# Kernel tuning notes

Hardware: AMD Instinct MI355X
Metric: run time of the kernel (lower is better)

Reference implementation:

```python
import jax, jax.numpy as jnp
import numpy as np

EMB = 768
HEADS = 12
HEAD_DIM = EMB // HEADS
SEQ = 4096
BATCH = 1


def setup_inputs() -> dict:
    key = jax.random.key(0)
    ks = jax.random.split(key, 9)
    s = 1.0 / np.sqrt(EMB)
    return {
        "x": jax.random.normal(ks[0], (BATCH, SEQ, EMB), dtype=jnp.float32),
        "wq": jax.random.normal(ks[1], (EMB, EMB), dtype=jnp.float32) * s,
        "bq": jax.random.normal(ks[2], (EMB,), dtype=jnp.float32) * s,
        "wk": jax.random.normal(ks[3], (EMB, EMB), dtype=jnp.float32) * s,
        "bk": jax.random.normal(ks[4], (EMB,), dtype=jnp.float32) * s,
        "wv": jax.random.normal(ks[5], (EMB, EMB), dtype=jnp.float32) * s,
        "bv": jax.random.normal(ks[6], (EMB,), dtype=jnp.float32) * s,
        "wo": jax.random.normal(ks[7], (EMB, EMB), dtype=jnp.float32) * s,
        "bo": jax.random.normal(ks[8], (EMB,), dtype=jnp.float32) * s,
    }


def reference(x, wq, bq, wk, bk, wv, bv, wo, bo):
    b, n, _ = x.shape
    # projections: [b, n, emb] -> [b, heads, n, head_dim]
    def split_heads(t):
        return t.reshape(b, n, HEADS, HEAD_DIM).transpose(0, 2, 1, 3)
    q = split_heads(x @ wq + bq)
    k = split_heads(x @ wk + bk)
    v = split_heads(x @ wv + bv)
    # full N x N scores (naive attention, as in the original)
    scores = jnp.einsum("bhqd,bhkd->bhqk", q, k)
    causal = jnp.triu(jnp.ones((n, n), dtype=bool), k=1)
    scores = jnp.where(causal, -jnp.inf, scores)
    weights = jax.nn.softmax(scores / np.sqrt(HEAD_DIM), axis=-1)
    # dropout with rate 0.0 is identity (eval mode)
    ctx = jnp.einsum("bhqk,bhkd->bhqd", weights, v)
    ctx = ctx.transpose(0, 2, 1, 3).reshape(b, n, EMB)
    return ctx @ wo + bo
```

## Files before the change

kernel.cpp:

```cpp
#include <hip/hip_runtime.h>
#include <stdint.h>

#define SEQ 4096
#define EMB 768
#define HEADS 12
#define HD 64

typedef __attribute__((ext_vector_type(8))) short short8;
typedef __attribute__((ext_vector_type(4))) short short4v;
typedef __attribute__((ext_vector_type(8))) __bf16 bf16x8;
typedef __attribute__((ext_vector_type(4))) __bf16 bf16x4;
typedef __attribute__((ext_vector_type(4))) float f32x4;

#define QSCALE 0.18033688011112043f

static __device__ __forceinline__ unsigned short f2bf(float f) {
    unsigned int u = __builtin_bit_cast(unsigned int, f);
    unsigned int r = 0x7fffu + ((u >> 16) & 1u);
    u += r;
    return (unsigned short)(u >> 16);
}

static __device__ __forceinline__ f32x4 mfma32(short8 a, short8 b, f32x4 c) {
    return __builtin_amdgcn_mfma_f32_16x16x32_bf16(
        __builtin_bit_cast(bf16x8, a), __builtin_bit_cast(bf16x8, b), c, 0, 0, 0);
}

static __device__ __forceinline__ f32x4 mfma16(short4v a, short4v b, f32x4 c) {
#if __has_builtin(__builtin_amdgcn_mfma_f32_16x16x16_bf16)
    return __builtin_amdgcn_mfma_f32_16x16x16_bf16(
        __builtin_bit_cast(bf16x4, a), __builtin_bit_cast(bf16x4, b), c, 0, 0, 0);
#else
    return __builtin_amdgcn_mfma_f32_16x16x16bf16_1k(a, b, c, 0, 0, 0);
#endif
}

static __device__ __forceinline__ short4v pack4bf(float a, float b, float c, float d) {
#if __has_builtin(__builtin_amdgcn_cvt_pk_bf16_f32)
    typedef __attribute__((ext_vector_type(2))) __bf16 bf16x2;
    bf16x2 lo = __builtin_amdgcn_cvt_pk_bf16_f32(a, b);
    bf16x2 hi = __builtin_amdgcn_cvt_pk_bf16_f32(c, d);
    uint2 u = {__builtin_bit_cast(unsigned int, lo), __builtin_bit_cast(unsigned int, hi)};
    return __builtin_bit_cast(short4v, u);
#else
    short4v p;
    p[0] = (short)f2bf(a); p[1] = (short)f2bf(b);
    p[2] = (short)f2bf(c); p[3] = (short)f2bf(d);
    return p;
#endif
}

static __device__ __forceinline__ void load_lds16(const void* g, void* l) {
    __builtin_amdgcn_global_load_lds(
        (const __attribute__((address_space(1))) unsigned int*)(uintptr_t)g,
        (__attribute__((address_space(3))) unsigned int*)(uintptr_t)l, 16, 0, 0);
}

static __device__ __forceinline__ int pid_of(int h, int i128, int ch) {
    int b = (i128 < 20) ? (i128 - 10)
                        : (i128 < 30 ? 10 + (i128 - 20) * 2 : 30 + (i128 - 30) * 3);
    return h * 36 + b + (ch - 1);
}

static __device__ __forceinline__ void softmax_step(f32x4* st, float& m_i, float& l_i,
                                                    f32x4* O, short4v* pk) {
    float t0 = fmaxf(fmaxf(st[0][0], st[0][1]), fmaxf(st[0][2], st[0][3]));
    float t1 = fmaxf(fmaxf(st[1][0], st[1][1]), fmaxf(st[1][2], st[1][3]));
    float t2 = fmaxf(fmaxf(st[2][0], st[2][1]), fmaxf(st[2][2], st[2][3]));
    float t3 = fmaxf(fmaxf(st[3][0], st[3][1]), fmaxf(st[3][2], st[3][3]));
    float mx = fmaxf(fmaxf(t0, t1), fmaxf(t2, t3));
    mx = fmaxf(mx, __shfl_xor(mx, 16));
    mx = fmaxf(mx, __shfl_xor(mx, 32));
    if (__ballot(mx > m_i + 5.0f)) {
        const bool inc = mx > m_i;
        const float mn = inc ? mx : m_i;
        const float alpha = __builtin_amdgcn_exp2f(m_i - mn);
        m_i = mn;
        l_i *= alpha;
        for (int dt = 0; dt < 4; dt++)
            for (int r = 0; r < 4; r++) O[dt][r] *= alpha;
    }
    float rs = 0.f;
    for (int nt = 0; nt < 4; nt++) {
        float p0 = __builtin_amdgcn_exp2f(st[nt][0] - m_i);
        float p1 = __builtin_amdgcn_exp2f(st[nt][1] - m_i);
        float p2 = __builtin_amdgcn_exp2f(st[nt][2] - m_i);
        float p3 = __builtin_amdgcn_exp2f(st[nt][3] - m_i);
        rs += p0 + p1 + p2 + p3;
        pk[nt] = pack4bf(p0, p1, p2, p3);
    }
    l_i += rs;
}

__global__ __launch_bounds__(256) void convert_all(const float* __restrict__ x,
                                                   const float* __restrict__ wq,
                                                   const float* __restrict__ wk,
                                                   const float* __restrict__ wv,
                                                   const float* __restrict__ wo,
                                                   unsigned short* __restrict__ xb,
                                                   unsigned short* __restrict__ wqkvT,
                                                   unsigned short* __restrict__ woT) {
    __shared__ float Ls[64][65];
    const int bid = blockIdx.x;
    if (bid < 3072) {
        int i = bid * 256 + threadIdx.x;
        float4 v = ((const float4*)x)[i];
        ushort4 o = {f2bf(v.x), f2bf(v.y), f2bf(v.z), f2bf(v.w)};
        ((ushort4*)xb)[i] = o;
        return;
    }
    const int idx = bid - 3072;
    const int z = idx / 144;
    const int bx = (idx % 144) / 12, by = idx % 12;
    const float* W = (z == 0) ? wq : (z == 1) ? wk : (z == 2) ? wv : wo;
    unsigned short* dst = (z < 3) ? (wqkvT + (size_t)z * EMB * EMB) : woT;
    const int k0 = bx * 64, n0 = by * 64;
    const int r = threadIdx.x >> 2, c0 = (threadIdx.x & 3) * 16;
    for (int j = 0; j < 16; j += 4) {
        float4 v = *(const float4*)&W[(size_t)(k0 + r) * EMB + n0 + c0 + j];
        Ls[r][c0 + j] = v.x;
        Ls[r][c0 + j + 1] = v.y;
        Ls[r][c0 + j + 2] = v.z;
        Ls[r][c0 + j + 3] = v.w;
    }
    __syncthreads();
    unsigned short tmp[16];
    for (int j = 0; j < 16; j++) tmp[j] = f2bf(Ls[c0 + j][r]);
    *(uint4*)&dst[(size_t)(n0 + r) * EMB + k0 + c0] = *(uint4*)tmp;
    *(uint4*)&dst[(size_t)(n0 + r) * EMB + k0 + c0 + 8] = *(uint4*)(tmp + 8);
}

__global__ __launch_bounds__(256) void gemm_qkv(const unsigned short* __restrict__ A,
                                                const unsigned short* __restrict__ Bt,
                                                const float* __restrict__ b0p,
                                                const float* __restrict__ b1p,
                                                const float* __restrict__ b2p,
                                                unsigned short* __restrict__ QKb,
                                                unsigned short* __restrict__ Vtb) {
    __shared__ __align__(16) unsigned short SMEM[16384];
    const int tid = threadIdx.x;
    const int wave = tid >> 6, lane = tid & 63, quad = lane >> 4, l16 = lane & 15;
    const int m0 = blockIdx.x * 128, n0 = blockIdx.y * 128;
    const int wm = (wave >> 1) * 64, wn = (wave & 1) * 64;
    const int lrow = lane >> 2, lcol = (lane & 3) * 8;

    f32x4 acc[4][4] = {};

    for (int t = 0; t < 2; t++) {
        int row = wave * 32 + t * 16 + lrow;
        load_lds16(&A[(size_t)(m0 + row) * EMB + lcol], &SMEM[(wave * 2 + t) * 512]);
        load_lds16(&Bt[(size_t)(n0 + row) * EMB + lcol], &SMEM[4096 + (wave * 2 + t) * 512]);
    }
    int buf = 0;
    for (int k0 = 0; k0 < EMB; k0 += 32) {
        __syncthreads();
        if (k0 + 32 < EMB) {
            unsigned short* A_ = &SMEM[(buf ^ 1) * 8192];
            unsigned short* B_ = A_ + 4096;
            for (int t = 0; t < 2; t++) {
                int row = wave * 32 + t * 16 + lrow;
                load_lds16(&A[(size_t)(m0 + row) * EMB + k0 + 32 + lcol], &A_[(wave * 2 + t) * 512]);
                load_lds16(&Bt[(size_t)(n0 + row) * EMB + k0 + 32 + lcol], &B_[(wave * 2 + t) * 512]);
            }
        }
        const unsigned short* A_ = &SMEM[buf * 8192];
        const unsigned short* B_ = A_ + 4096;
        short8 a[4], b[4];
        for (int i = 0; i < 4; i++) a[i] = *(const short8*)&A_[(wm + i * 16 + l16) * 32 + quad * 8];
        for (int i = 0; i < 4; i++) b[i] = *(const short8*)&B_[(wn + i * 16 + l16) * 32 + quad * 8];
        for (int i = 0; i < 4; i++)
            for (int j = 0; j < 4; j++) acc[i][j] = mfma32(a[i], b[j], acc[i][j]);
        buf ^= 1;
    }

    const int z = n0 / EMB;
    if (z < 2) {
        const float* bias = z ? b1p : b0p;
        const float sc = z ? 1.0f : QSCALE;
        for (int i = 0; i < 4; i++)
            for (int j = 0; j < 4; j++) {
                int mbase = m0 + wm + i * 16 + quad * 4;
                int n = n0 + wn + j * 16 + l16;
                float bv = bias[n - z * EMB];
                for (int r = 0; r < 4; r++)
                    QKb[(size_t)(mbase + r) * 1536 + n] = f2bf((acc[i][j][r] + bv) * sc);
            }
    } else {
        const int nn = n0 + wn + l16 - 2 * EMB;
        for (int j = 0; j < 4; j++) {
            __syncthreads();
            const float bv = b2p[nn + j * 16];
            const int nloc = (wave & 1) * 16 + l16;
            for (int i = 0; i < 4; i++) {
                ushort4 pk;
                pk.x = f2bf(acc[i][j][0] + bv);
                pk.y = f2bf(acc[i][j][1] + bv);
                pk.z = f2bf(acc[i][j][2] + bv);
                pk.w = f2bf(acc[i][j][3] + bv);
                *(ushort4*)&SMEM[nloc * 136 + wm + i * 16 + quad * 4] = pk;
            }
            __syncthreads();
            const int nl = tid >> 3, c = tid & 7;
            const int ng = (nl >> 4) * 64 + j * 16 + (nl & 15) + n0 - 2 * EMB;
            const int hh = ng >> 6, dd = ng & 63;
            unsigned short* dst = &Vtb[(size_t)(hh * HD + dd) * SEQ + m0];
            *(uint4*)&dst[c * 8] = *(uint4*)&SMEM[nl * 136 + c * 8];
            *(uint4*)&dst[64 + c * 8] = *(uint4*)&SMEM[nl * 136 + 64 + c * 8];
        }
    }
}

__global__ __launch_bounds__(256) void gemm_out(const unsigned short* __restrict__ A,
                                                const unsigned short* __restrict__ Bt,
                                                const float* __restrict__ bias,
                                                float* __restrict__ outp) {
    __shared__ __align__(16) unsigned short SMEM[12288];
    const int tid = threadIdx.x;
    const int wave = tid >> 6, lane = tid & 63, quad = lane >> 4, l16 = lane & 15;
    const int m0 = blockIdx.x * 64, n0 = blockIdx.y * 128;
    const int wm = (wave >> 1) * 32, wn = (wave & 1) * 64;
    const int lrow = lane >> 2, lcol = (lane & 3) * 8;

    f32x4 acc[2][4] = {};

    load_lds16(&A[(size_t)(m0 + wave * 16 + lrow) * EMB + lcol], &SMEM[wave * 512]);
    for (int t = 0; t < 2; t++) {
        int row = wave * 32 + t * 16 + lrow;
        load_lds16(&Bt[(size_t)(n0 + row) * EMB + lcol], &SMEM[4096 + (wave * 2 + t) * 512]);
    }
    int buf = 0;
    for (int k0 = 0; k0 < EMB; k0 += 32) {
        __syncthreads();
        if (k0 + 32 < EMB) {
            unsigned short* A_ = &SMEM[(buf ^ 1) * 2048];
            unsigned short* B_ = &SMEM[4096 + (buf ^ 1) * 4096];
            load_lds16(&A[(size_t)(m0 + wave * 16 + lrow) * EMB + k0 + 32 + lcol], &A_[wave * 512]);
            for (int t = 0; t < 2; t++) {
                int row = wave * 32 + t * 16 + lrow;
                load_lds16(&Bt[(size_t)(n0 + row) * EMB + k0 + 32 + lcol], &B_[(wave * 2 + t) * 512]);
            }
        }
        const unsigned short* A_ = &SMEM[buf * 2048];
        const unsigned short* B_ = &SMEM[4096 + buf * 4096];
        short8 a[2], b[4];
        for (int i = 0; i < 2; i++) a[i] = *(const short8*)&A_[(wm + i * 16 + l16) * 32 + quad * 8];
        for (int j = 0; j < 4; j++) b[j] = *(const short8*)&B_[(wn + j * 16 + l16) * 32 + quad * 8];
        for (int i = 0; i < 2; i++)
            for (int j = 0; j < 4; j++) acc[i][j] = mfma32(a[i], b[j], acc[i][j]);
        buf ^= 1;
    }

    for (int i = 0; i < 2; i++)
        for (int j = 0; j < 4; j++) {
            int mbase = m0 + wm + i * 16 + quad * 4;
            int n = n0 + wn + j * 16 + l16;
            float bv = bias[n];
            for (int r = 0; r < 4; r++) outp[(size_t)(mbase + r) * EMB + n] = acc[i][j][r] + bv;
        }
}

__global__ __launch_bounds__(512) void attn_kernel(const unsigned short* __restrict__ QKb,
                                                   const unsigned short* __restrict__ Vtb,
                                                   unsigned short* __restrict__ ctxb,
                                                   unsigned short* __restrict__ Op,
                                                   float* __restrict__ mArr,
                                                   float* __restrict__ lArr) {
    __shared__ __align__(16) unsigned short Ks[2][64 * 64];
    __shared__ __align__(16) unsigned short Vs[2][64 * 64];

    const int bid = blockIdx.x;
    const int h = bid % HEADS;
    const int r2 = 67 - bid / HEADS;
    int i128, ch, nch;
    if (r2 < 10) {
        i128 = r2; ch = 0; nch = 1;
    } else if (r2 < 30) {
        int t = r2 - 10; i128 = 10 + (t >> 1); ch = t & 1; nch = 2;
    } else if (r2 < 60) {
        int t = r2 - 30; i128 = 20 + t / 3; ch = t % 3; nch = 3;
    } else {
        int t = r2 - 60; i128 = 30 + (t >> 2); ch = t & 3; nch = 4;
    }
    const int T = 2 * i128 + 2;
    const int kb = ch * T / nch;
    const int ke = (ch + 1) * T / nch - 1;
    const int qbase = i128 * 128;
    const int tid = threadIdx.x;
    const int wave = tid >> 6, lane = tid & 63, quad = lane >> 4, l16 = lane & 15;

    const unsigned short* Qg = QKb + (size_t)h * HD;
    const unsigned short* Kg = QKb + (size_t)(EMB + h * HD);
    const unsigned short* Vh = Vtb + (size_t)h * HD * SEQ;

    const int q = qbase + wave * 16 + l16;
    const short8 bQ0 = *(const short8*)&Qg[(size_t)q * 1536 + quad * 8];
    const short8 bQ1 = *(const short8*)&Qg[(size_t)q * 1536 + 32 + quad * 8];

    const int row = tid >> 3, t8 = tid & 7;
    const int swk = row & 7, swv = row & 15;

    f32x4 O[4] = {};
    float m_i = -3.0e38f, l_i = 0.f;

    uint4 kr, vr;
    {
        const int kb64 = kb * 64;
        kr = *(const uint4*)&Kg[(size_t)(kb64 + row) * 1536 + t8 * 8];
        vr = *(const uint4*)&Vh[(size_t)row * SEQ + kb64 + t8 * 8];
    }
    *(uint4*)&Ks[0][row * 64 + (t8 ^ swk) * 8] = kr;
    *(uint2*)&Vs[0][row * 64 + ((2 * t8) ^ swv) * 4] = ((const uint2*)&vr)[0];
    *(uint2*)&Vs[0][row * 64 + ((2 * t8 + 1) ^ swv) * 4] = ((const uint2*)&vr)[1];
    if (kb < ke) {
        const int nb = (kb + 1) * 64;
        kr = *(const uint4*)&Kg[(size_t)(nb + row) * 1536 + t8 * 8];
        vr = *(const uint4*)&Vh[(size_t)row * SEQ + nb + t8 * 8];
    }
    __syncthreads();

    const int qw = qbase + wave * 16 + 15;
    int p = 0;
    for (int kt = kb; kt <= ke; kt++) {
        const int kbase = kt * 64;
        if (kt < ke) {
            const int pn = p ^ 1;
            *(uint4*)&Ks[pn][row * 64 + (t8 ^ swk) * 8] = kr;
            *(uint2*)&Vs[pn][row * 64 + ((2 * t8) ^ swv) * 4] = ((const uint2*)&vr)[0];
            *(uint2*)&Vs[pn][row * 64 + ((2 * t8 + 1) ^ swv) * 4] = ((const uint2*)&vr)[1];
            if (kt + 1 < ke) {
                const int nb = (kt + 2) * 64;
                kr = *(const uint4*)&Kg[(size_t)(nb + row) * 1536 + t8 * 8];
                vr = *(const uint4*)&Vh[(size_t)row * SEQ + nb + t8 * 8];
            }
        }

        if (kbase <= qw) {
            const int swr = l16 & 7;
            f32x4 st[4];
            for (int nt = 0; nt < 4; nt++) {
                short8 aK0 = *(const short8*)&Ks[p][(nt * 16 + l16) * 64 + (quad ^ swr) * 8];
                short8 aK1 = *(const short8*)&Ks[p][(nt * 16 + l16) * 64 + ((quad + 4) ^ swr) * 8];
                f32x4 z = {};
                z = mfma32(aK0, bQ0, z);
                z = mfma32(aK1, bQ1, z);
                st[nt] = z;
            }
            if (kbase + 63 > qbase + wave * 16) {
                for (int nt = 0; nt < 4; nt++)
                    for (int r = 0; r < 4; r++)
                        if (kbase + nt * 16 + quad * 4 + r > q) st[nt][r] = -INFINITY;
            }

            short4v pk[4];
            softmax_step(st, m_i, l_i, O, pk);

            for (int dt = 0; dt < 4; dt++)
                for (int nt = 0; nt < 4; nt++) {
                    short4v av =
                        *(const short4v*)&Vs[p][(dt * 16 + l16) * 64 + ((4 * nt + quad) ^ l16) * 4];
                    O[dt] = mfma16(av, pk[nt], O[dt]);
                }
        }

        __syncthreads();
        p ^= 1;
    }

    l_i += __shfl_xor(l_i, 16);
    l_i += __shfl_xor(l_i, 32);

    const int ql = wave * 16 + l16;
    if (nch == 1) {
        const float inv = 1.f / l_i;
        for (int dt = 0; dt < 4; dt++) {
            ushort4 o;
            o.x = f2bf(O[dt][0] * inv);
            o.y = f2bf(O[dt][1] * inv);
            o.z = f2bf(O[dt][2] * inv);
            o.w = f2bf(O[dt][3] * inv);
            *(ushort4*)&ctxb[(size_t)q * EMB + h * HD + dt * 16 + quad * 4] = o;
        }
    } else {
        if (ch == 0) {
            for (int dt = 0; dt < 4; dt++) {
                ushort4 o;
                o.x = f2bf(O[dt][0]);
                o.y = f2bf(O[dt][1]);
                o.z = f2bf(O[dt][2]);
                o.w = f2bf(O[dt][3]);
                *(ushort4*)&ctxb[(size_t)q * EMB + h * HD + dt * 16 + quad * 4] = o;
            }
        } else {
            const int pid = pid_of(h, i128, ch);
            for (int dt = 0; dt < 4; dt++) {
                ushort4 o;
                o.x = f2bf(O[dt][0]);
                o.y = f2bf(O[dt][1]);
                o.z = f2bf(O[dt][2]);
                o.w = f2bf(O[dt][3]);
                *(ushort4*)&Op[(size_t)pid * 8192 + ql * 64 + dt * 16 + quad * 4] = o;
            }
        }
        if (quad == 0) {
            const int mli = ((h * 32 + i128) * 4 + ch) * 128 + ql;
            mArr[mli] = m_i;
            lArr[mli] = l_i;
        }
    }
}

__global__ __launch_bounds__(256) void merge_kernel(const unsigned short* __restrict__ Op,
                                                    const float* __restrict__ mArr,
                                                    const float* __restrict__ lArr,
                                                    unsigned short* __restrict__ ctxb) {
    const int gid = blockIdx.x;
    const int h = gid % HEADS;
    const int i128 = 10 + gid / HEADS;
    const int nch = (i128 < 20) ? 2 : (i128 < 30) ? 3 : 4;
    const int q = threadIdx.x >> 1, d0 = (threadIdx.x & 1) * 32;
    const int mlbase = (h * 32 + i128) * 4;

    float mc[4], lc[4];
    for (int c = 0; c < nch; c++) {
        mc[c] = mArr[(mlbase + c) * 128 + q];
        lc[c] = lArr[(mlbase + c) * 128 + q];
    }
    float M = mc[0];
    for (int c = 1; c < nch; c++) M = fmaxf(M, mc[c]);
    float w[4], L = 0.f;
    for (int c = 0; c < nch; c++) {
        w[c] = __builtin_amdgcn_exp2f(mc[c] - M);
        L += w[c] * lc[c];
    }
    const float inv = 1.f / L;
    for (int c = 0; c < nch; c++) w[c] *= inv;

    unsigned short* dst = &ctxb[(size_t)(i128 * 128 + q) * EMB + h * HD + d0];
    for (int jj = 0; jj < 32; jj += 8) {
        uint4 u0 = *(const uint4*)&dst[jj];
        float f[8];
        const unsigned short* p0 = (const unsigned short*)&u0;
        for (int t = 0; t < 8; t++)
            f[t] = w[0] * __builtin_bit_cast(float, (unsigned int)p0[t] << 16);
        for (int c = 1; c < nch; c++) {
            const int pid = pid_of(h, i128, c);
            uint4 u = *(const uint4*)&Op[(size_t)pid * 8192 + q * 64 + d0 + jj];
            const unsigned short* p = (const unsigned short*)&u;
            for (int t = 0; t < 8; t++)
                f[t] += w[c] * __builtin_bit_cast(float, (unsigned int)p[t] << 16);
        }
        unsigned short o[8];
        for (int t = 0; t < 8; t++) o[t] = f2bf(f[t]);
        *(uint4*)&dst[jj] = *(uint4*)o;
    }
}

extern "C" void kernel_launch(void* const* d_in, const int* in_sizes, int n_in,
                              void* d_out, int out_size, void* d_ws, size_t ws_size,
                              hipStream_t stream) {
    const float* x = (const float*)d_in[0];
    const float* wq = (const float*)d_in[1];
    const float* bq = (const float*)d_in[2];
    const float* wk = (const float*)d_in[3];
    const float* bk = (const float*)d_in[4];
    const float* wv = (const float*)d_in[5];
    const float* bv = (const float*)d_in[6];
    const float* wo = (const float*)d_in[7];
    const float* bo = (const float*)d_in[8];

    unsigned short* ws = (unsigned short*)d_ws;
    unsigned short* xb = ws;
    unsigned short* wqkvT = xb + SEQ * EMB;
    unsigned short* woT = wqkvT + 3 * EMB * EMB;
    unsigned short* QKb = woT + EMB * EMB;
    unsigned short* Vtb = QKb + (size_t)SEQ * 1536;
    unsigned short* ctxb = Vtb + HEADS * SEQ * HD;
    unsigned short* Op = xb;
    float* mArr = (float*)(ws + 3538944);
    float* lArr = mArr + 196608;

    convert_all<<<dim3(3072 + 576), 256, 0, stream>>>(x, wq, wk, wv, wo, xb, wqkvT, woT);
    gemm_qkv<<<dim3(SEQ / 128, 3 * EMB / 128), 256, 0, stream>>>(
        xb, wqkvT, bq, bk, bv, QKb, Vtb);
    attn_kernel<<<dim3(12 * 68), 512, 0, stream>>>(QKb, Vtb, ctxb, Op, mArr, lArr);
    merge_kernel<<<dim3(264), 256, 0, stream>>>(Op, mArr, lArr, ctxb);
    gemm_out<<<dim3(SEQ / 64, EMB / 128), 256, 0, stream>>>(ctxb, woT, bo, (float*)d_out);
}
```

Baseline: 188.4 us.

## Process two 16-row query tiles per wave with 256-thread attention blocks

The attention kernel now uses 4 waves of 256 threads per block instead of 8 waves of 512. Each wave handles 32 query rows as two 16-row tiles, so every K and V fragment read from shared memory feeds two MFMA streams. This halves LDS reads per query and spreads the K/V tile loads over fewer threads. In exchange, each thread holds twice the accumulators and softmax state, which raises register pressure and could cut occupancy despite the launch_bounds(256,3) hint.

```diff
diff --git a/kernel.cpp b/kernel.cpp
--- a/kernel.cpp
+++ b/kernel.cpp
@@ -259,12 +259,12 @@
         }
 }
 
-__global__ __launch_bounds__(512) void attn_kernel(const unsigned short* __restrict__ QKb,
-                                                   const unsigned short* __restrict__ Vtb,
-                                                   unsigned short* __restrict__ ctxb,
-                                                   unsigned short* __restrict__ Op,
-                                                   float* __restrict__ mArr,
-                                                   float* __restrict__ lArr) {
+__global__ __launch_bounds__(256, 3) void attn_kernel(const unsigned short* __restrict__ QKb,
+                                                      const unsigned short* __restrict__ Vtb,
+                                                      unsigned short* __restrict__ ctxb,
+                                                      unsigned short* __restrict__ Op,
+                                                      float* __restrict__ mArr,
+                                                      float* __restrict__ lArr) {
     __shared__ __align__(16) unsigned short Ks[2][64 * 64];
     __shared__ __align__(16) unsigned short Vs[2][64 * 64];
 
@@ -292,73 +292,104 @@
     const unsigned short* Kg = QKb + (size_t)(EMB + h * HD);
     const unsigned short* Vh = Vtb + (size_t)h * HD * SEQ;
 
-    const int q = qbase + wave * 16 + l16;
-    const short8 bQ0 = *(const short8*)&Qg[(size_t)q * 1536 + quad * 8];
-    const short8 bQ1 = *(const short8*)&Qg[(size_t)q * 1536 + 32 + quad * 8];
-
-    const int row = tid >> 3, t8 = tid & 7;
+    const int qa = qbase + wave * 32 + l16;
+    const int qb = qa + 16;
+    const short8 bQ0a = *(const short8*)&Qg[(size_t)qa * 1536 + quad * 8];
+    const short8 bQ1a = *(const short8*)&Qg[(size_t)qa * 1536 + 32 + quad * 8];
+    const short8 bQ0b = *(const short8*)&Qg[(size_t)qb * 1536 + quad * 8];
+    const short8 bQ1b = *(const short8*)&Qg[(size_t)qb * 1536 + 32 + quad * 8];
+
+    const int row = tid >> 2, t4 = tid & 3;
     const int swk = row & 7, swv = row & 15;
 
-    f32x4 O[4] = {};
-    float m_i = -3.0e38f, l_i = 0.f;
-
-    uint4 kr, vr;
+    f32x4 Oa[4] = {}, Ob[4] = {};
+    float m_a = -3.0e38f, l_a = 0.f;
+    float m_b = -3.0e38f, l_b = 0.f;
+
+    uint4 kr0, kr1, vr0, vr1;
     {
         const int kb64 = kb * 64;
-        kr = *(const uint4*)&Kg[(size_t)(kb64 + row) * 1536 + t8 * 8];
-        vr = *(const uint4*)&Vh[(size_t)row * SEQ + kb64 + t8 * 8];
-    }
-    *(uint4*)&Ks[0][row * 64 + (t8 ^ swk) * 8] = kr;
-    *(uint2*)&Vs[0][row * 64 + ((2 * t8) ^ swv) * 4] = ((const uint2*)&vr)[0];
-    *(uint2*)&Vs[0][row * 64 + ((2 * t8 + 1) ^ swv) * 4] = ((const uint2*)&vr)[1];
+        const unsigned short* kp = &Kg[(size_t)(kb64 + row) * 1536];
+        kr0 = *(const uint4*)&kp[(2 * t4) * 8];
+        kr1 = *(const uint4*)&kp[(2 * t4 + 1) * 8];
+        const unsigned short* vp = &Vh[(size_t)row * SEQ + kb64];
+        vr0 = *(const uint4*)&vp[t4 * 16];
+        vr1 = *(const uint4*)&vp[t4 * 16 + 8];
+    }
+    *(uint4*)&Ks[0][row * 64 + ((2 * t4) ^ swk) * 8] = kr0;
+    *(uint4*)&Ks[0][row * 64 + ((2 * t4 + 1) ^ swk) * 8] = kr1;
+    *(uint2*)&Vs[0][row * 64 + ((4 * t4) ^ swv) * 4] = ((const uint2*)&vr0)[0];
+    *(uint2*)&Vs[0][row * 64 + ((4 * t4 + 1) ^ swv) * 4] = ((const uint2*)&vr0)[1];
+    *(uint2*)&Vs[0][row * 64 + ((4 * t4 + 2) ^ swv) * 4] = ((const uint2*)&vr1)[0];
+    *(uint2*)&Vs[0][row * 64 + ((4 * t4 + 3) ^ swv) * 4] = ((const uint2*)&vr1)[1];
     if (kb < ke) {
         const int nb = (kb + 1) * 64;
-        kr = *(const uint4*)&Kg[(size_t)(nb + row) * 1536 + t8 * 8];
-        vr = *(const uint4*)&Vh[(size_t)row * SEQ + nb + t8 * 8];
+        const unsigned short* kp = &Kg[(size_t)(nb + row) * 1536];
+        kr0 = *(const uint4*)&kp[(2 * t4) * 8];
+        kr1 = *(const uint4*)&kp[(2 * t4 + 1) * 8];
+        const unsigned short* vp = &Vh[(size_t)row * SEQ + nb];
+        vr0 = *(const uint4*)&vp[t4 * 16];
+        vr1 = *(const uint4*)&vp[t4 * 16 + 8];
     }
     __syncthreads();
 
-    const int qw = qbase + wave * 16 + 15;
+    const int qw = qbase + wave * 32 + 31;
     int p = 0;
     for (int kt = kb; kt <= ke; kt++) {
         const int kbase = kt * 64;
         if (kt < ke) {
             const int pn = p ^ 1;
-            *(uint4*)&Ks[pn][row * 64 + (t8 ^ swk) * 8] = kr;
-            *(uint2*)&Vs[pn][row * 64 + ((2 * t8) ^ swv) * 4] = ((const uint2*)&vr)[0];
-            *(uint2*)&Vs[pn][row * 64 + ((2 * t8 + 1) ^ swv) * 4] = ((const uint2*)&vr)[1];
+            *(uint4*)&Ks[pn][row * 64 + ((2 * t4) ^ swk) * 8] = kr0;
+            *(uint4*)&Ks[pn][row * 64 + ((2 * t4 + 1) ^ swk) * 8] = kr1;
+            *(uint2*)&Vs[pn][row * 64 + ((4 * t4) ^ swv) * 4] = ((const uint2*)&vr0)[0];
+            *(uint2*)&Vs[pn][row * 64 + ((4 * t4 + 1) ^ swv) * 4] = ((const uint2*)&vr0)[1];
+            *(uint2*)&Vs[pn][row * 64 + ((4 * t4 + 2) ^ swv) * 4] = ((const uint2*)&vr1)[0];
+            *(uint2*)&Vs[pn][row * 64 + ((4 * t4 + 3) ^ swv) * 4] = ((const uint2*)&vr1)[1];
             if (kt + 1 < ke) {
                 const int nb = (kt + 2) * 64;
-                kr = *(const uint4*)&Kg[(size_t)(nb + row) * 1536 + t8 * 8];
-                vr = *(const uint4*)&Vh[(size_t)row * SEQ + nb + t8 * 8];
+                const unsigned short* kp = &Kg[(size_t)(nb + row) * 1536];
+                kr0 = *(const uint4*)&kp[(2 * t4) * 8];
+                kr1 = *(const uint4*)&kp[(2 * t4 + 1) * 8];
+                const unsigned short* vp = &Vh[(size_t)row * SEQ + nb];
+                vr0 = *(const uint4*)&vp[t4 * 16];
+                vr1 = *(const uint4*)&vp[t4 * 16 + 8];
             }
         }
 
         if (kbase <= qw) {
             const int swr = l16 & 7;
-            f32x4 st[4];
+            f32x4 sa[4], sb[4];
             for (int nt = 0; nt < 4; nt++) {
                 short8 aK0 = *(const short8*)&Ks[p][(nt * 16 + l16) * 64 + (quad ^ swr) * 8];
                 short8 aK1 = *(const short8*)&Ks[p][(nt * 16 + l16) * 64 + ((quad + 4) ^ swr) * 8];
-                f32x4 z = {};
-                z = mfma32(aK0, bQ0, z);
-                z = mfma32(aK1, bQ1, z);
-                st[nt] = z;
-            }
-            if (kbase + 63 > qbase + wave * 16) {
+                f32x4 za = {};
+                za = mfma32(aK0, bQ0a, za);
+                za = mfma32(aK1, bQ1a, za);
+                sa[nt] = za;
+                f32x4 zb = {};
+                zb = mfma32(aK0, bQ0b, zb);
+                zb = mfma32(aK1, bQ1b, zb);
+                sb[nt] = zb;
+            }
+            if (kbase + 63 > qbase + wave * 32) {
                 for (int nt = 0; nt < 4; nt++)
-                    for (int r = 0; r < 4; r++)
-                        if (kbase + nt * 16 + quad * 4 + r > q) st[nt][r] = -INFINITY;
-            }
-
-            short4v pk[4];
-            softmax_step(st, m_i, l_i, O, pk);
+                    for (int r = 0; r < 4; r++) {
+                        const int kk = kbase + nt * 16 + quad * 4 + r;
+                        if (kk > qa) sa[nt][r] = -INFINITY;
+                        if (kk > qb) sb[nt][r] = -INFINITY;
+                    }
+            }
+
+            short4v pka[4], pkb[4];
+            softmax_step(sa, m_a, l_a, Oa, pka);
+            softmax_step(sb, m_b, l_b, Ob, pkb);
 
             for (int dt = 0; dt < 4; dt++)
                 for (int nt = 0; nt < 4; nt++) {
                     short4v av =
                         *(const short4v*)&Vs[p][(dt * 16 + l16) * 64 + ((4 * nt + quad) ^ l16) * 4];
-                    O[dt] = mfma16(av, pk[nt], O[dt]);
+                    Oa[dt] = mfma16(av, pka[nt], Oa[dt]);
+                    Ob[dt] = mfma16(av, pkb[nt], Ob[dt]);
                 }
         }
 
@@ -366,45 +397,65 @@
         p ^= 1;
     }
 
-    l_i += __shfl_xor(l_i, 16);
-    l_i += __shfl_xor(l_i, 32);
-
-    const int ql = wave * 16 + l16;
+    l_a += __shfl_xor(l_a, 16);
+    l_a += __shfl_xor(l_a, 32);
+    l_b += __shfl_xor(l_b, 16);
+    l_b += __shfl_xor(l_b, 32);
+
+    const int qla = wave * 32 + l16;
+    const int qlb = qla + 16;
     if (nch == 1) {
-        const float inv = 1.f / l_i;
+        const float ia = 1.f / l_a, ib = 1.f / l_b;
         for (int dt = 0; dt < 4; dt++) {
-            ushort4 o;
-            o.x = f2bf(O[dt][0] * inv);
-            o.y = f2bf(O[dt][1] * inv);
-            o.z = f2bf(O[dt][2] * inv);
-            o.w = f2bf(O[dt][3] * inv);
-            *(ushort4*)&ctxb[(size_t)q * EMB + h * HD + dt * 16 + quad * 4] = o;
+            ushort4 oa, ob;
+            oa.x = f2bf(Oa[dt][0] * ia);
+            oa.y = f2bf(Oa[dt][1] * ia);
+            oa.z = f2bf(Oa[dt][2] * ia);
+            oa.w = f2bf(Oa[dt][3] * ia);
+            ob.x = f2bf(Ob[dt][0] * ib);
+            ob.y = f2bf(Ob[dt][1] * ib);
+            ob.z = f2bf(Ob[dt][2] * ib);
+            ob.w = f2bf(Ob[dt][3] * ib);
+            *(ushort4*)&ctxb[(size_t)qa * EMB + h * HD + dt * 16 + quad * 4] = oa;
+            *(ushort4*)&ctxb[(size_t)qb * EMB + h * HD + dt * 16 + quad * 4] = ob;
         }
     } else {
         if (ch == 0) {
             for (int dt = 0; dt < 4; dt++) {
-                ushort4 o;
-                o.x = f2bf(O[dt][0]);
-                o.y = f2bf(O[dt][1]);
-                o.z = f2bf(O[dt][2]);
-                o.w = f2bf(O[dt][3]);
-                *(ushort4*)&ctxb[(size_t)q * EMB + h * HD + dt * 16 + quad * 4] = o;
+                ushort4 oa, ob;
+                oa.x = f2bf(Oa[dt][0]);
+                oa.y = f2bf(Oa[dt][1]);
+                oa.z = f2bf(Oa[dt][2]);
+                oa.w = f2bf(Oa[dt][3]);
+                ob.x = f2bf(Ob[dt][0]);
+                ob.y = f2bf(Ob[dt][1]);
+                ob.z = f2bf(Ob[dt][2]);
+                ob.w = f2bf(Ob[dt][3]);
+                *(ushort4*)&ctxb[(size_t)qa * EMB + h * HD + dt * 16 + quad * 4] = oa;
+                *(ushort4*)&ctxb[(size_t)qb * EMB + h * HD + dt * 16 + quad * 4] = ob;
             }
         } else {
             const int pid = pid_of(h, i128, ch);
             for (int dt = 0; dt < 4; dt++) {
-                ushort4 o;
-                o.x = f2bf(O[dt][0]);
-                o.y = f2bf(O[dt][1]);
-                o.z = f2bf(O[dt][2]);
-                o.w = f2bf(O[dt][3]);
-                *(ushort4*)&Op[(size_t)pid * 8192 + ql * 64 + dt * 16 + quad * 4] = o;
+                ushort4 oa, ob;
+                oa.x = f2bf(Oa[dt][0]);
+                oa.y = f2bf(Oa[dt][1]);
+                oa.z = f2bf(Oa[dt][2]);
+                oa.w = f2bf(Oa[dt][3]);
+                ob.x = f2bf(Ob[dt][0]);
+                ob.y = f2bf(Ob[dt][1]);
+                ob.z = f2bf(Ob[dt][2]);
+                ob.w = f2bf(Ob[dt][3]);
+                *(ushort4*)&Op[(size_t)pid * 8192 + qla * 64 + dt * 16 + quad * 4] = oa;
+                *(ushort4*)&Op[(size_t)pid * 8192 + qlb * 64 + dt * 16 + quad * 4] = ob;
             }
         }
         if (quad == 0) {
-            const int mli = ((h * 32 + i128) * 4 + ch) * 128 + ql;
-            mArr[mli] = m_i;
-            lArr[mli] = l_i;
+            const int mlb = ((h * 32 + i128) * 4 + ch) * 128;
+            mArr[mlb + qla] = m_a;
+            lArr[mlb + qla] = l_a;
+            mArr[mlb + qlb] = m_b;
+            lArr[mlb + qlb] = l_b;
         }
     }
 }
@@ -482,7 +533,7 @@
     convert_all<<<dim3(3072 + 576), 256, 0, stream>>>(x, wq, wk, wv, wo, xb, wqkvT, woT);
     gemm_qkv<<<dim3(SEQ / 128, 3 * EMB / 128), 256, 0, stream>>>(
         xb, wqkvT, bq, bk, bv, QKb, Vtb);
-    attn_kernel<<<dim3(12 * 68), 512, 0, stream>>>(QKb, Vtb, ctxb, Op, mArr, lArr);
+    attn_kernel<<<dim3(12 * 68), 256, 0, stream>>>(QKb, Vtb, ctxb, Op, mArr, lArr);
     merge_kernel<<<dim3(264), 256, 0, stream>>>(Op, mArr, lArr, ctxb);
     gemm_out<<<dim3(SEQ / 64, EMB / 128), 256, 0, stream>>>(ctxb, woT, bo, (float*)d_out);
 }
```

Result: no change. 186.3 us (-1.1%).
